# Kernel optimization log

Measured on AMD Instinct MI355X. Metric: run time of the kernel, lower is better.

Reference implementation:

```python
import jax, jax.numpy as jnp
import numpy as np

VOCAB = 8192  # upper bound on integer values appearing in features


def setup_inputs() -> dict:
    key = jax.random.key(0)
    # [B, L] integer codes; each row is treated as a SET of values (duplicates ignored)
    features = jax.random.randint(key, (4096, 256), 0, VOCAB, dtype=jnp.int32)
    return {"features": features}


def reference(features) -> jnp.ndarray:
    # np.intersect1d / np.union1d compute set intersection/union of unique values.
    # Equivalent vectorized form: binary presence matrix P[i, v] = 1 iff value v in row i.
    B, L = features.shape
    rows = jnp.arange(B)[:, None]                                  # [B, 1]
    presence = jnp.zeros((B, VOCAB), jnp.float32).at[rows, features].set(1.0)  # [B, V]
    inter = presence @ presence.T                                  # [B, B] |A_i & A_j|
    sizes = presence.sum(axis=1)                                   # [B]    |A_i|
    union = sizes[:, None] + sizes[None, :] - inter                # [B, B] |A_i | A_j|
    # original returns -intersection/union (note the negation), 0 when union == 0
    sim = jnp.where(union != 0, -inter / jnp.where(union != 0, union, 1.0), 0.0)
    return sim
```

## Files before the change

kernel.cpp:

```cpp
#include <hip/hip_runtime.h>
#include <hip/hip_bf16.h>
#include <stdint.h>

#define B_ROWS 4096
#define L_FEAT 256
#define VOCAB  8192

#define BM 128
#define BN 128
#define BK 64

typedef __attribute__((ext_vector_type(4))) int   intx4;
typedef __attribute__((ext_vector_type(4))) float floatx4;

__device__ __forceinline__ void async_copy16(const void* gsrc, void* ldst) {
  __builtin_amdgcn_global_load_lds(
      (const __attribute__((address_space(1))) void*)gsrc,
      (__attribute__((address_space(3))) void*)ldst, 16, 0, 0);
}

__global__ void zero_kernel(uint4* __restrict__ p, int n16) {
  int i = blockIdx.x * blockDim.x + threadIdx.x;
  const int stride = gridDim.x * blockDim.x;
  const uint4 z = make_uint4(0u, 0u, 0u, 0u);
  for (; i < n16; i += stride) p[i] = z;
}

__global__ void scatter_kernel(const int* __restrict__ f,
                               unsigned char* __restrict__ P) {
  const int id  = blockIdx.x * 256 + threadIdx.x;
  const int row = id >> 8;
  const int v   = f[id];
  P[(size_t)row * VOCAB + v] = 1;
}

__global__ void sizes_kernel(const uint4* __restrict__ P4,
                             float* __restrict__ sizes) {
  const int row = blockIdx.x;
  const uint4* rp = P4 + (size_t)row * (VOCAB / 16);
  int cnt = 0;
  for (int j = threadIdx.x; j < VOCAB / 16; j += 256) {
    uint4 x = rp[j];
    cnt += __popc(x.x) + __popc(x.y) + __popc(x.z) + __popc(x.w);
  }
  #pragma unroll
  for (int off = 32; off > 0; off >>= 1) cnt += __shfl_down(cnt, off);
  __shared__ int ws[4];
  if ((threadIdx.x & 63) == 0) ws[threadIdx.x >> 6] = cnt;
  __syncthreads();
  if (threadIdx.x == 0)
    sizes[row] = (float)(ws[0] + ws[1] + ws[2] + ws[3]);
}

__global__ __launch_bounds__(256) void gemm_kernel(
    const unsigned char* __restrict__ P,
    const float* __restrict__ sizes,
    float* __restrict__ out) {
  int b = blockIdx.x, by = 0, rem = 32;
  while (b >= rem) { b -= rem; ++by; --rem; }
  const int bx = by + b;
  const int iBase = by * BM;
  const int jBase = bx * BN;

  __shared__ __align__(16) unsigned char As[BM * BK];
  __shared__ __align__(16) unsigned char Bs[BN * BK];

  const int tid  = threadIdx.x;
  const int wave = tid >> 6, lane = tid & 63;
  const int wm = wave >> 1, wn = wave & 1;
  const int col16 = lane & 15, quad = lane >> 4;

  intx4 acc[4][4];
  #pragma unroll
  for (int a = 0; a < 4; ++a)
    #pragma unroll
    for (int c = 0; c < 4; ++c) acc[a][c] = (intx4){0, 0, 0, 0};

  const int srow = lane >> 2;
  const int scol = (lane & 3) * 16;

  for (int k0 = 0; k0 < VOCAB; k0 += BK) {
    __syncthreads();
    #pragma unroll
    for (int t = 0; t < 2; ++t) {
      const int c = wave + t * 4;
      const int r = c * 16 + srow;
      async_copy16(P + (size_t)(iBase + r) * VOCAB + k0 + scol, &As[c * 1024]);
      async_copy16(P + (size_t)(jBase + r) * VOCAB + k0 + scol, &Bs[c * 1024]);
    }
    __syncthreads();

    intx4 a[4], bfr[4];
    #pragma unroll
    for (int tm = 0; tm < 4; ++tm)
      a[tm] = *(const intx4*)&As[(wm * 64 + tm * 16 + col16) * BK + quad * 16];
    #pragma unroll
    for (int tn = 0; tn < 4; ++tn)
      bfr[tn] = *(const intx4*)&Bs[(wn * 64 + tn * 16 + col16) * BK + quad * 16];
    #pragma unroll
    for (int tm = 0; tm < 4; ++tm)
      #pragma unroll
      for (int tn = 0; tn < 4; ++tn)
        acc[tm][tn] = __builtin_amdgcn_mfma_i32_16x16x64_i8(
            a[tm], bfr[tn], acc[tm][tn], 0, 0, 0);
  }

  #pragma unroll
  for (int tm = 0; tm < 4; ++tm) {
    #pragma unroll
    for (int tn = 0; tn < 4; ++tn) {
      const int col = jBase + wn * 64 + tn * 16 + col16;
      const float sj = sizes[col];
      #pragma unroll
      for (int r = 0; r < 4; ++r) {
        const int row = iBase + wm * 64 + tm * 16 + quad * 4 + r;
        const float inter = (float)acc[tm][tn][r];
        const float u = sizes[row] + sj - inter;
        out[(size_t)row * B_ROWS + col] = (u != 0.f) ? (-inter / u) : 0.f;
      }
    }
  }
}

__global__ void mirror_kernel(float* __restrict__ out) {
  const int bx = blockIdx.x, by = blockIdx.y;
  if (bx >= by) return;
  const int rBase = by * 128, cBase = bx * 128;
  __shared__ float tile[32][33];
  const int tx = threadIdx.x & 31, ty8 = threadIdx.x >> 5;
  for (int s = 0; s < 16; ++s) {
    const int si = s >> 2, sj = s & 3;
    #pragma unroll
    for (int k = 0; k < 4; ++k) {
      const int sr = ty8 + k * 8;
      tile[sr][tx] =
          out[(size_t)(cBase + sj * 32 + sr) * B_ROWS + rBase + si * 32 + tx];
    }
    __syncthreads();
    #pragma unroll
    for (int k = 0; k < 4; ++k) {
      const int dr = ty8 + k * 8;
      out[(size_t)(rBase + si * 32 + dr) * B_ROWS + cBase + sj * 32 + tx] =
          tile[tx][dr];
    }
    __syncthreads();
  }
}

extern "C" void kernel_launch(void* const* d_in, const int* in_sizes, int n_in,
                              void* d_out, int out_size, void* d_ws, size_t ws_size,
                              hipStream_t stream) {
  const int* features = (const int*)d_in[0];
  float* out = (float*)d_out;
  unsigned char* P = (unsigned char*)d_ws;
  float* sizes = (float*)((char*)d_ws + (size_t)B_ROWS * VOCAB);

  zero_kernel<<<2048, 256, 0, stream>>>((uint4*)P, B_ROWS * VOCAB / 16);
  scatter_kernel<<<(B_ROWS * L_FEAT) / 256, 256, 0, stream>>>(features, P);
  sizes_kernel<<<B_ROWS, 256, 0, stream>>>((const uint4*)P, sizes);
  gemm_kernel<<<528, 256, 0, stream>>>(P, sizes, out);
  mirror_kernel<<<dim3(32, 32), 256, 0, stream>>>(out);
}
```

Measured before the change: 199.7 us.

## Fuse presence build, double-buffer GEMM with LDS swizzle, write symmetric output directly

```diff
diff --git a/kernel.cpp b/kernel.cpp
--- a/kernel.cpp
+++ b/kernel.cpp
@@ -19,37 +19,38 @@
       (__attribute__((address_space(3))) void*)ldst, 16, 0, 0);
 }
 
-__global__ void zero_kernel(uint4* __restrict__ p, int n16) {
-  int i = blockIdx.x * blockDim.x + threadIdx.x;
-  const int stride = gridDim.x * blockDim.x;
+__global__ __launch_bounds__(256) void presence_kernel(
+    const int* __restrict__ f,
+    unsigned char* __restrict__ P,
+    float* __restrict__ sizes) {
+  __shared__ __align__(16) unsigned char row_p[VOCAB];
+  const int row = blockIdx.x;
+  const int tid = threadIdx.x;
+
+  uint4* rp4 = (uint4*)row_p;
   const uint4 z = make_uint4(0u, 0u, 0u, 0u);
-  for (; i < n16; i += stride) p[i] = z;
-}
+  #pragma unroll
+  for (int j = 0; j < 2; ++j) rp4[tid + j * 256] = z;
+  __syncthreads();
 
-__global__ void scatter_kernel(const int* __restrict__ f,
-                               unsigned char* __restrict__ P) {
-  const int id  = blockIdx.x * 256 + threadIdx.x;
-  const int row = id >> 8;
-  const int v   = f[id];
-  P[(size_t)row * VOCAB + v] = 1;
-}
+  const int v = f[row * L_FEAT + tid];
+  row_p[v] = 1;
+  __syncthreads();
 
-__global__ void sizes_kernel(const uint4* __restrict__ P4,
-                             float* __restrict__ sizes) {
-  const int row = blockIdx.x;
-  const uint4* rp = P4 + (size_t)row * (VOCAB / 16);
   int cnt = 0;
-  for (int j = threadIdx.x; j < VOCAB / 16; j += 256) {
-    uint4 x = rp[j];
+  uint4* op4 = (uint4*)(P + (size_t)row * VOCAB);
+  #pragma unroll
+  for (int j = 0; j < 2; ++j) {
+    const uint4 x = rp4[tid + j * 256];
+    op4[tid + j * 256] = x;
     cnt += __popc(x.x) + __popc(x.y) + __popc(x.z) + __popc(x.w);
   }
   #pragma unroll
   for (int off = 32; off > 0; off >>= 1) cnt += __shfl_down(cnt, off);
   __shared__ int ws[4];
-  if ((threadIdx.x & 63) == 0) ws[threadIdx.x >> 6] = cnt;
+  if ((tid & 63) == 0) ws[tid >> 6] = cnt;
   __syncthreads();
-  if (threadIdx.x == 0)
-    sizes[row] = (float)(ws[0] + ws[1] + ws[2] + ws[3]);
+  if (tid == 0) sizes[row] = (float)(ws[0] + ws[1] + ws[2] + ws[3]);
 }
 
 __global__ __launch_bounds__(256) void gemm_kernel(
@@ -62,8 +63,8 @@
   const int iBase = by * BM;
   const int jBase = bx * BN;
 
-  __shared__ __align__(16) unsigned char As[BM * BK];
-  __shared__ __align__(16) unsigned char Bs[BN * BK];
+  __shared__ __align__(16) unsigned char As[2][BM * BK];
+  __shared__ __align__(16) unsigned char Bs[2][BN * BK];
 
   const int tid  = threadIdx.x;
   const int wave = tid >> 6, lane = tid & 63;
@@ -77,73 +78,85 @@
     for (int c = 0; c < 4; ++c) acc[a][c] = (intx4){0, 0, 0, 0};
 
   const int srow = lane >> 2;
-  const int scol = (lane & 3) * 16;
+  const int scol = ((lane & 3) ^ ((lane >> 3) & 3)) * 16;
 
-  for (int k0 = 0; k0 < VOCAB; k0 += BK) {
-    __syncthreads();
-    #pragma unroll
-    for (int t = 0; t < 2; ++t) {
-      const int c = wave + t * 4;
-      const int r = c * 16 + srow;
-      async_copy16(P + (size_t)(iBase + r) * VOCAB + k0 + scol, &As[c * 1024]);
-      async_copy16(P + (size_t)(jBase + r) * VOCAB + k0 + scol, &Bs[c * 1024]);
+  #define STAGE(buf, k0)                                                      \
+    {                                                                         \
+      _Pragma("unroll")                                                       \
+      for (int t = 0; t < 2; ++t) {                                           \
+        const int c = wave + t * 4;                           \
+        const int r = c * 16 + srow;                     \
+        async_copy16(P + (size_t)(iBase + r) * VOCAB + (k0) + scol,           \
+                     &As[buf][c * 1024]);                                     \
+        async_copy16(P + (size_t)(jBase + r) * VOCAB + (k0) + scol,           \
+                     &Bs[buf][c * 1024]);                                     \
+      }                                                                       \
     }
-    __syncthreads();
+
+  STAGE(0, 0);
+  __syncthreads();
+
+  const int sw = (col16 >> 1) & 3;
+
+  int cur = 0;
+  for (int k0 = 0; k0 < VOCAB; k0 += BK, cur ^= 1) {
+    if (k0 + BK < VOCAB) STAGE(cur ^ 1, k0 + BK);
 
     intx4 a[4], bfr[4];
     #pragma unroll
     for (int tm = 0; tm < 4; ++tm)
-      a[tm] = *(const intx4*)&As[(wm * 64 + tm * 16 + col16) * BK + quad * 16];
+      a[tm] = *(const intx4*)&As[cur][(wm * 64 + tm * 16 + col16) * BK +
+                                      (quad ^ sw) * 16];
     #pragma unroll
     for (int tn = 0; tn < 4; ++tn)
-      bfr[tn] = *(const intx4*)&Bs[(wn * 64 + tn * 16 + col16) * BK + quad * 16];
+      bfr[tn] = *(const intx4*)&Bs[cur][(wn * 64 + tn * 16 + col16) * BK +
+                                        (quad ^ sw) * 16];
     #pragma unroll
     for (int tm = 0; tm < 4; ++tm)
       #pragma unroll
       for (int tn = 0; tn < 4; ++tn)
         acc[tm][tn] = __builtin_amdgcn_mfma_i32_16x16x64_i8(
             a[tm], bfr[tn], acc[tm][tn], 0, 0, 0);
+
+    __syncthreads();
   }
 
   #pragma unroll
   for (int tm = 0; tm < 4; ++tm) {
+    const int rowb = iBase + wm * 64 + tm * 16 + quad * 4;
+    const float si0 = sizes[rowb + 0], si1 = sizes[rowb + 1];
+    const float si2 = sizes[rowb + 2], si3 = sizes[rowb + 3];
     #pragma unroll
     for (int tn = 0; tn < 4; ++tn) {
       const int col = jBase + wn * 64 + tn * 16 + col16;
       const float sj = sizes[col];
-      #pragma unroll
-      for (int r = 0; r < 4; ++r) {
-        const int row = iBase + wm * 64 + tm * 16 + quad * 4 + r;
-        const float inter = (float)acc[tm][tn][r];
-        const float u = sizes[row] + sj - inter;
-        out[(size_t)row * B_ROWS + col] = (u != 0.f) ? (-inter / u) : 0.f;
+      floatx4 tv;
+      {
+        const float inter = (float)acc[tm][tn][0];
+        const float u = si0 + sj - inter;
+        tv[0] = (u != 0.f) ? (-inter / u) : 0.f;
       }
+      {
+        const float inter = (float)acc[tm][tn][1];
+        const float u = si1 + sj - inter;
+        tv[1] = (u != 0.f) ? (-inter / u) : 0.f;
+      }
+      {
+        const float inter = (float)acc[tm][tn][2];
+        const float u = si2 + sj - inter;
+        tv[2] = (u != 0.f) ? (-inter / u) : 0.f;
+      }
+      {
+        const float inter = (float)acc[tm][tn][3];
+        const float u = si3 + sj - inter;
+        tv[3] = (u != 0.f) ? (-inter / u) : 0.f;
+      }
+      out[(size_t)(rowb + 0) * B_ROWS + col] = tv[0];
+      out[(size_t)(rowb + 1) * B_ROWS + col] = tv[1];
+      out[(size_t)(rowb + 2) * B_ROWS + col] = tv[2];
+      out[(size_t)(rowb + 3) * B_ROWS + col] = tv[3];
+      *(floatx4*)&out[(size_t)col * B_ROWS + rowb] = tv;
     }
-  }
-}
-
-__global__ void mirror_kernel(float* __restrict__ out) {
-  const int bx = blockIdx.x, by = blockIdx.y;
-  if (bx >= by) return;
-  const int rBase = by * 128, cBase = bx * 128;
-  __shared__ float tile[32][33];
-  const int tx = threadIdx.x & 31, ty8 = threadIdx.x >> 5;
-  for (int s = 0; s < 16; ++s) {
-    const int si = s >> 2, sj = s & 3;
-    #pragma unroll
-    for (int k = 0; k < 4; ++k) {
-      const int sr = ty8 + k * 8;
-      tile[sr][tx] =
-          out[(size_t)(cBase + sj * 32 + sr) * B_ROWS + rBase + si * 32 + tx];
-    }
-    __syncthreads();
-    #pragma unroll
-    for (int k = 0; k < 4; ++k) {
-      const int dr = ty8 + k * 8;
-      out[(size_t)(rBase + si * 32 + dr) * B_ROWS + cBase + sj * 32 + tx] =
-          tile[tx][dr];
-    }
-    __syncthreads();
   }
 }
 
@@ -155,9 +168,6 @@
   unsigned char* P = (unsigned char*)d_ws;
   float* sizes = (float*)((char*)d_ws + (size_t)B_ROWS * VOCAB);
 
-  zero_kernel<<<2048, 256, 0, stream>>>((uint4*)P, B_ROWS * VOCAB / 16);
-  scatter_kernel<<<(B_ROWS * L_FEAT) / 256, 256, 0, stream>>>(features, P);
-  sizes_kernel<<<B_ROWS, 256, 0, stream>>>((const uint4*)P, sizes);
+  presence_kernel<<<B_ROWS, 256, 0, stream>>>(features, P, sizes);
   gemm_kernel<<<528, 256, 0, stream>>>(P, sizes, out);
-  mirror_kernel<<<dim3(32, 32), 256, 0, stream>>>(out);
 }
```

Measured after the change: 185.2 us. 7.2% less time.
